# Performance work log

Measured on AMD Instinct MI355X. Metric: run time of the kernel, lower is better.

Reference implementation:

```python
import jax, jax.numpy as jnp
import numpy as np

MARGIN = 0.2
ALPHA = 2.0
BETA = 1.5
ANGLE_THRESHOLD = 30.0
EPS_PD = 1e-6   # F.pairwise_distance eps
EPS_CS = 1e-8   # F.cosine_similarity eps
NEG_INF = -1e30
POS_INF = 1e30


def setup_inputs() -> dict:
    key = jax.random.key(0)
    k1, k2, k3 = jax.random.split(key, 3)
    B, F, A = 4096, 512, 3
    features = jax.random.normal(k1, (B, F), dtype=jnp.float32)
    labels = jax.random.randint(k2, (B,), 0, 256)
    angles = jax.random.uniform(k3, (B, A), dtype=jnp.float32) * 90.0  # degrees
    features_orig = jax.random.normal(jax.random.fold_in(key, 7), (B, F), dtype=jnp.float32)
    return {"features": features, "labels": labels, "angles": angles, "features_orig": features_orig}


def _cosine_sim_matrix(f):
    norms = jnp.linalg.norm(f, axis=1)
    denom = jnp.maximum(norms[:, None] * norms[None, :], EPS_CS)
    return (f @ f.T) / denom


def _forward(features, labels, angles, features_orig):
    B = features.shape[0]
    idx = jnp.arange(B)
    # pairwise angle distances [B,B] (torch.cdist p=2)
    adist = jnp.sqrt(jnp.sum((angles[:, None, :] - angles[None, :, :]) ** 2, axis=-1))
    same = labels[:, None] == labels[None, :]
    same = same & ~jnp.eye(B, dtype=bool)          # exclude self
    diff = labels[:, None] != labels[None, :]
    has_pos = same.any(axis=1)
    has_neg = diff.any(axis=1)
    valid = has_pos & has_neg
    # hardest positive: same label, largest angle difference
    pos_idx = jnp.argmax(jnp.where(same, adist, NEG_INF), axis=1)
    # hardest negative: among diff-label within angle threshold, most similar feature;
    # else diff-label with smallest angle difference
    sim = _cosine_sim_matrix(features)
    similar = diff & (adist < ANGLE_THRESHOLD)
    sim_any = similar.any(axis=1)
    neg_idx_hard = jnp.argmax(jnp.where(similar, sim, NEG_INF), axis=1)
    neg_idx_far = jnp.argmin(jnp.where(diff, adist, POS_INF), axis=1)
    neg_idx = jnp.where(sim_any, neg_idx_hard, neg_idx_far)
    # triplet distances (F.pairwise_distance adds eps to the diff)
    a = features
    p = features[pos_idx]
    n = features[neg_idx]
    pos_d = jnp.linalg.norm(a - p + EPS_PD, axis=1)
    neg_d = jnp.linalg.norm(a - n + EPS_PD, axis=1)
    # angle-based weights (non-differentiable, matches .item() in torch)
    pa = adist[idx, pos_idx]
    na = adist[idx, neg_idx]
    w = jnp.where(pa > 45.0, ALPHA, 1.0) * jnp.where(na < 15.0, BETA, 1.0)
    basic = jax.nn.relu(pos_d - neg_d + MARGIN)
    vmask = valid.astype(features.dtype)
    cnt = jnp.maximum(vmask.sum(), 1.0)
    triplet_loss = jnp.sum(w * basic * vmask) / cnt
    # reconstruction term
    num = jnp.sum(features * features_orig, axis=1)
    den = jnp.maximum(jnp.linalg.norm(features, axis=1) * jnp.linalg.norm(features_orig, axis=1), EPS_CS)
    recon = 1.0 - jnp.mean(num / den)
    return triplet_loss + 0.1 * recon


def reference(features, labels, angles, features_orig):
    return _forward(features, labels, angles, features_orig)
```

## Files before the change

### kernel.cpp

```cpp
#include <hip/hip_runtime.h>
#include <math.h>

#define BN 4096
#define FD 512
#define TT 128
#define TJ 64
#define BK 64
#define NJT (BN / TT)
#define NPAIR (NJT * (NJT + 1) / 2)
#define NBLK (NPAIR * 2)
#define NPC 128

typedef __attribute__((ext_vector_type(8))) __bf16 bf16x8;
typedef __attribute__((ext_vector_type(4))) float floatx4;
typedef unsigned long long u64;

__device__ __forceinline__ float wred_sum(float v) {
#pragma unroll
  for (int m = 1; m < 64; m <<= 1) v += __shfl_xor(v, m, 64);
  return v;
}

__device__ __forceinline__ float dot4(float4 a, float4 b) {
  return a.x * b.x + a.y * b.y + a.z * b.z + a.w * b.w;
}

__device__ __forceinline__ unsigned short f2bf(float x) {
  unsigned u = __float_as_uint(x);
  u += 0x7fffu + ((u >> 16) & 1u);
  return (unsigned short)(u >> 16);
}

__device__ __forceinline__ void load16(const void* g, void* l) {
  __builtin_amdgcn_global_load_lds(
      (const __attribute__((address_space(1))) unsigned int*)g,
      (__attribute__((address_space(3))) unsigned int*)l, 16, 0, 0);
}

__device__ __forceinline__ unsigned ford(float v) {
  unsigned u = __float_as_uint(v);
  return u ^ (((unsigned)((int)u >> 31)) | 0x80000000u);
}

template <int N>
__device__ __forceinline__ int rori(int x) {
  return __builtin_amdgcn_update_dpp(0, x, 0x120 | N, 0xf, 0xf, true);
}
template <int N>
__device__ __forceinline__ u64 ror16_u64(u64 k) {
  unsigned lo = (unsigned)rori<N>((int)(unsigned)k);
  unsigned hi = (unsigned)rori<N>((int)(unsigned)(k >> 32));
  return ((u64)hi << 32) | lo;
}
__device__ __forceinline__ u64 red16_max_u64(u64 k) {
  u64 o;
  o = ror16_u64<1>(k); k = o > k ? o : k;
  o = ror16_u64<2>(k); k = o > k ? o : k;
  o = ror16_u64<4>(k); k = o > k ? o : k;
  o = ror16_u64<8>(k); k = o > k ? o : k;
  return k;
}

__device__ __forceinline__ u64 sx64(u64 v, int m) {
  unsigned lo = (unsigned)__shfl_xor((int)(unsigned)v, m, 64);
  unsigned hi = (unsigned)__shfl_xor((int)(unsigned)(v >> 32), m, 64);
  return ((u64)hi << 32) | lo;
}

__global__ __launch_bounds__(256) void k_prep(const float* __restrict__ f,
                                              const float* __restrict__ fo,
                                              const float* __restrict__ angles,
                                              unsigned short* __restrict__ gb,
                                              float* __restrict__ rowr,
                                              float* __restrict__ ax,
                                              float* __restrict__ ay,
                                              float* __restrict__ az) {
  const int i = blockIdx.x * 4 + (threadIdx.x >> 6);
  const int lane = threadIdx.x & 63;
  const int t = blockIdx.x * 256 + threadIdx.x;
  if (t < BN) {
    ax[t] = angles[t * 3 + 0];
    ay[t] = angles[t * 3 + 1];
    az[t] = angles[t * 3 + 2];
  }
  const float4* fr = (const float4*)(f + (size_t)i * FD);
  const float4* orr = (const float4*)(fo + (size_t)i * FD);
  float4 x0 = fr[lane], x1 = fr[lane + 64];
  float4 y0 = orr[lane], y1 = orr[lane + 64];
  float sff = dot4(x0, x0) + dot4(x1, x1);
  float sfo = dot4(x0, y0) + dot4(x1, y1);
  float soo = dot4(y0, y0) + dot4(y1, y1);
  sff = wred_sum(sff);
  sfo = wred_sum(sfo);
  soo = wred_sum(soo);
  float nf = sqrtf(sff);
  float inv = 1.0f / nf;
  ushort4* gr = (ushort4*)(gb + (size_t)i * FD);
  ushort4 s0, s1;
  s0.x = f2bf(x0.x * inv); s0.y = f2bf(x0.y * inv);
  s0.z = f2bf(x0.z * inv); s0.w = f2bf(x0.w * inv);
  s1.x = f2bf(x1.x * inv); s1.y = f2bf(x1.y * inv);
  s1.z = f2bf(x1.z * inv); s1.w = f2bf(x1.w * inv);
  gr[lane] = s0;
  gr[lane + 64] = s1;
  if (lane == 0) {
    rowr[i] = sfo / fmaxf(nf * sqrtf(soo), 1e-8f);
  }
}

__global__ __launch_bounds__(256, 4) void k_sim(const unsigned short* __restrict__ gb,
                                                const int* __restrict__ labels,
                                                const float* __restrict__ ax,
                                                const float* __restrict__ ay,
                                                const float* __restrict__ az,
                                                u64* __restrict__ pkey) {
  __shared__ unsigned short As[TT * BK];
  __shared__ unsigned short Bs[TJ * BK];
  const int h = blockIdx.x & 1;
  int a = 0, rem = blockIdx.x >> 1;
#pragma unroll 1
  while (rem >= NJT - a) { rem -= NJT - a; a++; }
  const int b = a + rem;
  const int i0 = a * TT;
  const int j0 = b * TT + h * TJ;

  const int tid = threadIdx.x;
  const int w = tid >> 6;
  const int lane = tid & 63;

  floatx4 acc[2][4];
#pragma unroll
  for (int u = 0; u < 2; u++)
#pragma unroll
    for (int v = 0; v < 4; v++) acc[u][v] = (floatx4){0.f, 0.f, 0.f, 0.f};

  const int rp = tid >> 3;
  const int q8 = ((tid & 7) ^ (rp & 7)) * 8;
  const unsigned short* gA[4];
  const unsigned short* gB[2];
  unsigned short* lA[4];
  unsigned short* lB[2];
#pragma unroll
  for (int c = 0; c < 4; c++) {
    gA[c] = gb + (size_t)(i0 + rp + 32 * c) * FD + q8;
    lA[c] = As + (tid + 256 * c) * 8;
  }
#pragma unroll
  for (int c = 0; c < 2; c++) {
    gB[c] = gb + (size_t)(j0 + rp + 32 * c) * FD + q8;
    lB[c] = Bs + (tid + 256 * c) * 8;
  }

  const int m = lane & 15;
  const int arow = w * 32 + m;
  const int brow = m;
  const int g4 = lane >> 4;
  const int l7 = lane & 7;
  const int koff0 = (g4 ^ l7) * 8;
  const int koff1 = ((4 + g4) ^ l7) * 8;

  for (int kc = 0; kc < FD; kc += BK) {
#pragma unroll
    for (int c = 0; c < 4; c++) load16(gA[c] + kc, lA[c]);
#pragma unroll
    for (int c = 0; c < 2; c++) load16(gB[c] + kc, lB[c]);
    __syncthreads();
    bf16x8 af[2], bf[4];
#pragma unroll
    for (int u = 0; u < 2; u++)
      af[u] = *(const bf16x8*)(As + (arow + u * 16) * BK + koff0);
#pragma unroll
    for (int v = 0; v < 4; v++)
      bf[v] = *(const bf16x8*)(Bs + (brow + v * 16) * BK + koff0);
#pragma unroll
    for (int u = 0; u < 2; u++)
#pragma unroll
      for (int v = 0; v < 4; v++)
        acc[u][v] = __builtin_amdgcn_mfma_f32_16x16x32_bf16(af[u], bf[v], acc[u][v], 0, 0, 0);
#pragma unroll
    for (int u = 0; u < 2; u++)
      af[u] = *(const bf16x8*)(As + (arow + u * 16) * BK + koff1);
#pragma unroll
    for (int v = 0; v < 4; v++)
      bf[v] = *(const bf16x8*)(Bs + (brow + v * 16) * BK + koff1);
#pragma unroll
    for (int u = 0; u < 2; u++)
#pragma unroll
      for (int v = 0; v < 4; v++)
        acc[u][v] = __builtin_amdgcn_mfma_f32_16x16x32_bf16(af[u], bf[v], acc[u][v], 0, 0, 0);
    __syncthreads();
  }

  const int quad = lane >> 4;
  const int cx = lane & 15;
  int jc[4], lj[4];
  float jx[4], jy[4], jz[4];
#pragma unroll
  for (int v = 0; v < 4; v++) {
    jc[v] = j0 + v * 16 + cx;
    lj[v] = labels[jc[v]];
    jx[v] = ax[jc[v]];
    jy[v] = ay[jc[v]];
    jz[v] = az[jc[v]];
  }
  const size_t rbase = (size_t)(64 + 2 * b + h) * BN;
  u64 ckey[4] = {0, 0, 0, 0};
#pragma unroll
  for (int u = 0; u < 2; u++) {
#pragma unroll
    for (int reg = 0; reg < 4; reg++) {
      int i = i0 + w * 32 + u * 16 + quad * 4 + reg;
      int li = labels[i];
      float a0 = ax[i], a1 = ay[i], a2 = az[i];
      u64 rkey = 0;
      unsigned ni = (unsigned)(~i);
#pragma unroll
      for (int v = 0; v < 4; v++) {
        float d0 = a0 - jx[v];
        float d1 = a1 - jy[v];
        float d2 = a2 - jz[v];
        float dd = d0 * d0 + d1 * d1 + d2 * d2;
        bool ok = (li != lj[v]) && (dd < 900.0f);
        u64 vh = (u64)ford(acc[u][v][reg]) << 32;
        u64 candR = vh | (unsigned)(~jc[v]);
        if (ok && candR > rkey) rkey = candR;
        u64 candC = vh | ni;
        if (ok && candC > ckey[v]) ckey[v] = candC;
      }
      rkey = red16_max_u64(rkey);
      if (cx == 0) pkey[rbase + i] = rkey;
    }
  }
  if (a != b) {
    const size_t cbase = (size_t)(4 * a + w) * BN;
#pragma unroll
    for (int v = 0; v < 4; v++) {
      u64 k = ckey[v];
      u64 o = sx64(k, 16); if (o > k) k = o;
      o = sx64(k, 32); if (o > k) k = o;
      if (quad == 0) pkey[cbase + jc[v]] = k;
    }
  }
}

__global__ __launch_bounds__(256) void k_final(const float* __restrict__ f,
                                               const int* __restrict__ labels,
                                               const float* __restrict__ ax,
                                               const float* __restrict__ ay,
                                               const float* __restrict__ az,
                                               const u64* __restrict__ pkey,
                                               float* __restrict__ rowc,
                                               float* __restrict__ rowv) {
  const int i = blockIdx.x * 4 + (threadIdx.x >> 6);
  const int lane = threadIdx.x & 63;
  const int li = labels[i];
  const float a0 = ax[i], a1 = ay[i], a2 = az[i];

  u64 keyP = 0;
  u64 keyN = ~0ull;
  const float4* ax4 = (const float4*)ax;
  const float4* ay4 = (const float4*)ay;
  const float4* az4 = (const float4*)az;
  const int4* lb4 = (const int4*)labels;
#pragma unroll
  for (int it = 0; it < 16; it++) {
    int bb = it * 64 + lane;
    float4 X = ax4[bb], Y = ay4[bb], Z = az4[bb];
    int4 L = lb4[bb];
    int jb = bb * 4;
#pragma unroll
    for (int s = 0; s < 4; s++) {
      float xx = s == 0 ? X.x : s == 1 ? X.y : s == 2 ? X.z : X.w;
      float yy = s == 0 ? Y.x : s == 1 ? Y.y : s == 2 ? Y.z : Y.w;
      float zz = s == 0 ? Z.x : s == 1 ? Z.y : s == 2 ? Z.z : Z.w;
      int ll = s == 0 ? L.x : s == 1 ? L.y : s == 2 ? L.z : L.w;
      int j = jb + s;
      float d0 = a0 - xx, d1 = a1 - yy, d2 = a2 - zz;
      float dd = d0 * d0 + d1 * d1 + d2 * d2;
      if (ll == li) {
        u64 kp = ((u64)__float_as_uint(dd) << 32) | (unsigned)(~j);
        if (j != i && kp > keyP) keyP = kp;
      } else {
        u64 kn = ((u64)__float_as_uint(dd) << 32) | (unsigned)j;
        if (kn < keyN) keyN = kn;
      }
    }
  }
  const int t = i >> 7;
  u64 s0 = (lane < 4 * t) ? pkey[(size_t)lane * BN + i] : 0;
  u64 s1 = (lane >= 2 * t) ? pkey[(size_t)(64 + lane) * BN + i] : 0;
  u64 keyS = s0 > s1 ? s0 : s1;
#pragma unroll
  for (int off = 1; off < 64; off <<= 1) {
    u64 o = sx64(keyP, off);
    if (o > keyP) keyP = o;
    o = sx64(keyN, off);
    if (o < keyN) keyN = o;
    o = sx64(keyS, off);
    if (o > keyS) keyS = o;
  }
  bool hp = keyP != 0;
  bool hn = keyN != ~0ull;
  if (!(hp && hn)) {
    if (lane == 0) { rowc[i] = 0.0f; rowv[i] = 0.0f; }
    return;
  }
  bool sim_any = keyS != 0;
  int pos = (int)(~(unsigned)keyP);
  int neg = sim_any ? (int)(~(unsigned)keyS) : (int)(unsigned)keyN;

  const float4* fa = (const float4*)(f + (size_t)i * FD);
  const float4* fp = (const float4*)(f + (size_t)pos * FD);
  const float4* fn = (const float4*)(f + (size_t)neg * FD);
  float sp = 0.0f, sn = 0.0f;
#pragma unroll
  for (int t2 = 0; t2 < 2; t2++) {
    float4 xa = fa[lane + t2 * 64];
    float4 xp = fp[lane + t2 * 64];
    float4 xn = fn[lane + t2 * 64];
    float dp;
    dp = xa.x - xp.x + 1e-6f; sp += dp * dp;
    dp = xa.y - xp.y + 1e-6f; sp += dp * dp;
    dp = xa.z - xp.z + 1e-6f; sp += dp * dp;
    dp = xa.w - xp.w + 1e-6f; sp += dp * dp;
    dp = xa.x - xn.x + 1e-6f; sn += dp * dp;
    dp = xa.y - xn.y + 1e-6f; sn += dp * dp;
    dp = xa.z - xn.z + 1e-6f; sn += dp * dp;
    dp = xa.w - xn.w + 1e-6f; sn += dp * dp;
  }
  sp = wred_sum(sp);
  sn = wred_sum(sn);

  if (lane == 0) {
    float pos_d = sqrtf(sp);
    float neg_d = sqrtf(sn);
    float pa = sqrtf(__uint_as_float((unsigned)(keyP >> 32)));
    float n0 = a0 - ax[neg];
    float n1 = a1 - ay[neg];
    float n2 = a2 - az[neg];
    float na = sqrtf(n0 * n0 + n1 * n1 + n2 * n2);
    float w = (pa > 45.0f ? 2.0f : 1.0f) * (na < 15.0f ? 1.5f : 1.0f);
    float basic = fmaxf(pos_d - neg_d + 0.2f, 0.0f);
    rowc[i] = w * basic;
    rowv[i] = 1.0f;
  }
}

__global__ __launch_bounds__(1024) void k_out(const float* __restrict__ rowc,
                                              const float* __restrict__ rowv,
                                              const float* __restrict__ rowr,
                                              float* __restrict__ out) {
  __shared__ float sc[16], sv[16], sr[16];
  const int t = threadIdx.x;
  float c = 0.0f, v = 0.0f, r = 0.0f;
  for (int i = t; i < BN; i += 1024) {
    c += rowc[i];
    v += rowv[i];
    r += rowr[i];
  }
  c = wred_sum(c);
  v = wred_sum(v);
  r = wred_sum(r);
  const int wid = t >> 6;
  if ((t & 63) == 0) { sc[wid] = c; sv[wid] = v; sr[wid] = r; }
  __syncthreads();
  if (t == 0) {
    float C = 0.0f, V = 0.0f, R = 0.0f;
#pragma unroll
    for (int k = 0; k < 16; k++) { C += sc[k]; V += sv[k]; R += sr[k]; }
    float tri = C / fmaxf(V, 1.0f);
    float recon = 1.0f - R / (float)BN;
    out[0] = tri + 0.1f * recon;
  }
}

extern "C" void kernel_launch(void* const* d_in, const int* in_sizes, int n_in,
                              void* d_out, int out_size, void* d_ws, size_t ws_size,
                              hipStream_t stream) {
  const float* feat = (const float*)d_in[0];
  const int* labels = (const int*)d_in[1];
  const float* angles = (const float*)d_in[2];
  const float* forig = (const float*)d_in[3];
  float* out = (float*)d_out;

  char* ws = (char*)d_ws;
  unsigned short* gb = (unsigned short*)ws;
  size_t off = (size_t)BN * FD * sizeof(unsigned short);
  u64* pkey = (u64*)(ws + off);     off += (size_t)NPC * BN * 8;
  float* rowc = (float*)(ws + off); off += (size_t)BN * 4;
  float* rowv = (float*)(ws + off); off += (size_t)BN * 4;
  float* rowr = (float*)(ws + off); off += (size_t)BN * 4;
  float* ax = (float*)(ws + off);   off += (size_t)BN * 4;
  float* ay = (float*)(ws + off);   off += (size_t)BN * 4;
  float* az = (float*)(ws + off);   off += (size_t)BN * 4;

  k_prep<<<BN / 4, 256, 0, stream>>>(feat, forig, angles, gb, rowr, ax, ay, az);
  k_sim<<<NBLK, 256, 0, stream>>>(gb, labels, ax, ay, az, pkey);
  k_final<<<BN / 4, 256, 0, stream>>>(feat, labels, ax, ay, az, pkey, rowc, rowv);
  k_out<<<1, 1024, 0, stream>>>(rowc, rowv, rowr, out);
}
```

Before: 108.6 us.

## Bucket rows by label, defer negative scan, fuse final reduction into k_final

Builds per-label buckets (a count histogram in k_prep plus a single-block prefix-scan/scatter kernel) so the hardest-positive search in k_final visits only same-label rows instead of all 4096. The nearest-negative full scan now runs only when no similar negative exists, and has_pos/has_neg come from bucket counts. The separate k_out reduction is folded into k_final using per-block partials and a last-block atomic counter. In exchange it adds a memset, a serial single-block kernel launch, global atomics, and scattered gathers of angle data through the bucket indices.

```diff
diff --git a/kernel.cpp b/kernel.cpp
--- a/kernel.cpp
+++ b/kernel.cpp
@@ -10,6 +10,7 @@
 #define NPAIR (NJT * (NJT + 1) / 2)
 #define NBLK (NPAIR * 2)
 #define NPC 128
+#define NFB (BN / 4)
 
 typedef __attribute__((ext_vector_type(8))) __bf16 bf16x8;
 typedef __attribute__((ext_vector_type(4))) float floatx4;
@@ -70,11 +71,13 @@
 __global__ __launch_bounds__(256) void k_prep(const float* __restrict__ f,
                                               const float* __restrict__ fo,
                                               const float* __restrict__ angles,
+                                              const int* __restrict__ labels,
                                               unsigned short* __restrict__ gb,
                                               float* __restrict__ rowr,
                                               float* __restrict__ ax,
                                               float* __restrict__ ay,
-                                              float* __restrict__ az) {
+                                              float* __restrict__ az,
+                                              int* __restrict__ cntP) {
   const int i = blockIdx.x * 4 + (threadIdx.x >> 6);
   const int lane = threadIdx.x & 63;
   const int t = blockIdx.x * 256 + threadIdx.x;
@@ -83,6 +86,7 @@
     ay[t] = angles[t * 3 + 1];
     az[t] = angles[t * 3 + 2];
   }
+  if (lane == 0) atomicAdd(&cntP[labels[i] * 16], 1);
   const float4* fr = (const float4*)(f + (size_t)i * FD);
   const float4* orr = (const float4*)(fo + (size_t)i * FD);
   float4 x0 = fr[lane], x1 = fr[lane + 64];
@@ -108,6 +112,36 @@
   }
 }
 
+__global__ __launch_bounds__(256) void k_bucket(const int* __restrict__ labels,
+                                                const int* __restrict__ cntP,
+                                                int* __restrict__ curP,
+                                                int* __restrict__ offc,
+                                                int* __restrict__ cntc,
+                                                int* __restrict__ bucket) {
+  __shared__ int pre[256];
+  const int tid = threadIdx.x;
+  int c = cntP[tid * 16];
+  pre[tid] = c;
+  __syncthreads();
+#pragma unroll
+  for (int s = 1; s < 256; s <<= 1) {
+    int v = (tid >= s) ? pre[tid - s] : 0;
+    __syncthreads();
+    pre[tid] += v;
+    __syncthreads();
+  }
+  int excl = pre[tid] - c;
+  offc[tid] = excl;
+  cntc[tid] = c;
+  curP[tid * 16] = excl;
+  __syncthreads();
+  for (int i = tid; i < BN; i += 256) {
+    int lab = labels[i];
+    int pos = atomicAdd(&curP[lab * 16], 1);
+    bucket[pos] = i;
+  }
+}
+
 __global__ __launch_bounds__(256, 4) void k_sim(const unsigned short* __restrict__ gb,
                                                 const int* __restrict__ labels,
                                                 const float* __restrict__ ax,
@@ -249,41 +283,33 @@
                                                const float* __restrict__ ay,
                                                const float* __restrict__ az,
                                                const u64* __restrict__ pkey,
-                                               float* __restrict__ rowc,
-                                               float* __restrict__ rowv) {
-  const int i = blockIdx.x * 4 + (threadIdx.x >> 6);
+                                               const float* __restrict__ rowr,
+                                               const int* __restrict__ bucket,
+                                               const int* __restrict__ offc,
+                                               const int* __restrict__ cntc,
+                                               float* __restrict__ blkC,
+                                               float* __restrict__ blkV,
+                                               float* __restrict__ blkR,
+                                               int* __restrict__ counter,
+                                               float* __restrict__ out) {
+  __shared__ float s_c[4], s_v[4], s_r[4];
+  __shared__ int s_go;
+  const int wid = threadIdx.x >> 6;
+  const int i = blockIdx.x * 4 + wid;
   const int lane = threadIdx.x & 63;
   const int li = labels[i];
   const float a0 = ax[i], a1 = ay[i], a2 = az[i];
 
+  const int bc = cntc[li];
+  const int bo = offc[li];
   u64 keyP = 0;
-  u64 keyN = ~0ull;
-  const float4* ax4 = (const float4*)ax;
-  const float4* ay4 = (const float4*)ay;
-  const float4* az4 = (const float4*)az;
-  const int4* lb4 = (const int4*)labels;
-#pragma unroll
-  for (int it = 0; it < 16; it++) {
-    int bb = it * 64 + lane;
-    float4 X = ax4[bb], Y = ay4[bb], Z = az4[bb];
-    int4 L = lb4[bb];
-    int jb = bb * 4;
-#pragma unroll
-    for (int s = 0; s < 4; s++) {
-      float xx = s == 0 ? X.x : s == 1 ? X.y : s == 2 ? X.z : X.w;
-      float yy = s == 0 ? Y.x : s == 1 ? Y.y : s == 2 ? Y.z : Y.w;
-      float zz = s == 0 ? Z.x : s == 1 ? Z.y : s == 2 ? Z.z : Z.w;
-      int ll = s == 0 ? L.x : s == 1 ? L.y : s == 2 ? L.z : L.w;
-      int j = jb + s;
-      float d0 = a0 - xx, d1 = a1 - yy, d2 = a2 - zz;
+  for (int l = lane; l < bc; l += 64) {
+    int j = bucket[bo + l];
+    if (j != i) {
+      float d0 = a0 - ax[j], d1 = a1 - ay[j], d2 = a2 - az[j];
       float dd = d0 * d0 + d1 * d1 + d2 * d2;
-      if (ll == li) {
-        u64 kp = ((u64)__float_as_uint(dd) << 32) | (unsigned)(~j);
-        if (j != i && kp > keyP) keyP = kp;
-      } else {
-        u64 kn = ((u64)__float_as_uint(dd) << 32) | (unsigned)j;
-        if (kn < keyN) keyN = kn;
-      }
+      u64 kp = ((u64)__float_as_uint(dd) << 32) | (unsigned)(~j);
+      if (kp > keyP) keyP = kp;
     }
   }
   const int t = i >> 7;
@@ -294,83 +320,122 @@
   for (int off = 1; off < 64; off <<= 1) {
     u64 o = sx64(keyP, off);
     if (o > keyP) keyP = o;
-    o = sx64(keyN, off);
-    if (o < keyN) keyN = o;
     o = sx64(keyS, off);
     if (o > keyS) keyS = o;
   }
-  bool hp = keyP != 0;
-  bool hn = keyN != ~0ull;
-  if (!(hp && hn)) {
-    if (lane == 0) { rowc[i] = 0.0f; rowv[i] = 0.0f; }
-    return;
-  }
+  bool hp = bc > 1;
+  bool hn = bc < BN;
   bool sim_any = keyS != 0;
-  int pos = (int)(~(unsigned)keyP);
-  int neg = sim_any ? (int)(~(unsigned)keyS) : (int)(unsigned)keyN;
-
-  const float4* fa = (const float4*)(f + (size_t)i * FD);
-  const float4* fp = (const float4*)(f + (size_t)pos * FD);
-  const float4* fn = (const float4*)(f + (size_t)neg * FD);
-  float sp = 0.0f, sn = 0.0f;
-#pragma unroll
-  for (int t2 = 0; t2 < 2; t2++) {
-    float4 xa = fa[lane + t2 * 64];
-    float4 xp = fp[lane + t2 * 64];
-    float4 xn = fn[lane + t2 * 64];
-    float dp;
-    dp = xa.x - xp.x + 1e-6f; sp += dp * dp;
-    dp = xa.y - xp.y + 1e-6f; sp += dp * dp;
-    dp = xa.z - xp.z + 1e-6f; sp += dp * dp;
-    dp = xa.w - xp.w + 1e-6f; sp += dp * dp;
-    dp = xa.x - xn.x + 1e-6f; sn += dp * dp;
-    dp = xa.y - xn.y + 1e-6f; sn += dp * dp;
-    dp = xa.z - xn.z + 1e-6f; sn += dp * dp;
-    dp = xa.w - xn.w + 1e-6f; sn += dp * dp;
-  }
-  sp = wred_sum(sp);
-  sn = wred_sum(sn);
-
+  float rc = 0.0f, rv = 0.0f;
+  if (hp && hn) {
+    int neg;
+    if (sim_any) {
+      neg = (int)(~(unsigned)keyS);
+    } else {
+      u64 keyN = ~0ull;
+      const float4* ax4 = (const float4*)ax;
+      const float4* ay4 = (const float4*)ay;
+      const float4* az4 = (const float4*)az;
+      const int4* lb4 = (const int4*)labels;
+      for (int it = 0; it < 16; it++) {
+        int bb = it * 64 + lane;
+        float4 X = ax4[bb], Y = ay4[bb], Z = az4[bb];
+        int4 L = lb4[bb];
+        int jb = bb * 4;
+#pragma unroll
+        for (int s = 0; s < 4; s++) {
+          float xx = s == 0 ? X.x : s == 1 ? X.y : s == 2 ? X.z : X.w;
+          float yy = s == 0 ? Y.x : s == 1 ? Y.y : s == 2 ? Y.z : Y.w;
+          float zz = s == 0 ? Z.x : s == 1 ? Z.y : s == 2 ? Z.z : Z.w;
+          int ll = s == 0 ? L.x : s == 1 ? L.y : s == 2 ? L.z : L.w;
+          int j = jb + s;
+          if (ll != li) {
+            float d0 = a0 - xx, d1 = a1 - yy, d2 = a2 - zz;
+            float dd = d0 * d0 + d1 * d1 + d2 * d2;
+            u64 kn = ((u64)__float_as_uint(dd) << 32) | (unsigned)j;
+            if (kn < keyN) keyN = kn;
+          }
+        }
+      }
+#pragma unroll
+      for (int off = 1; off < 64; off <<= 1) {
+        u64 o = sx64(keyN, off);
+        if (o < keyN) keyN = o;
+      }
+      neg = (int)(unsigned)keyN;
+    }
+    int pos = (int)(~(unsigned)keyP);
+
+    const float4* fa = (const float4*)(f + (size_t)i * FD);
+    const float4* fp = (const float4*)(f + (size_t)pos * FD);
+    const float4* fn = (const float4*)(f + (size_t)neg * FD);
+    float sp = 0.0f, sn = 0.0f;
+#pragma unroll
+    for (int t2 = 0; t2 < 2; t2++) {
+      float4 xa = fa[lane + t2 * 64];
+      float4 xp = fp[lane + t2 * 64];
+      float4 xn = fn[lane + t2 * 64];
+      float dp;
+      dp = xa.x - xp.x + 1e-6f; sp += dp * dp;
+      dp = xa.y - xp.y + 1e-6f; sp += dp * dp;
+      dp = xa.z - xp.z + 1e-6f; sp += dp * dp;
+      dp = xa.w - xp.w + 1e-6f; sp += dp * dp;
+      dp = xa.x - xn.x + 1e-6f; sn += dp * dp;
+      dp = xa.y - xn.y + 1e-6f; sn += dp * dp;
+      dp = xa.z - xn.z + 1e-6f; sn += dp * dp;
+      dp = xa.w - xn.w + 1e-6f; sn += dp * dp;
+    }
+    sp = wred_sum(sp);
+    sn = wred_sum(sn);
+    if (lane == 0) {
+      float pos_d = sqrtf(sp);
+      float neg_d = sqrtf(sn);
+      float pa = sqrtf(__uint_as_float((unsigned)(keyP >> 32)));
+      float n0 = a0 - ax[neg];
+      float n1 = a1 - ay[neg];
+      float n2 = a2 - az[neg];
+      float na = sqrtf(n0 * n0 + n1 * n1 + n2 * n2);
+      float w = (pa > 45.0f ? 2.0f : 1.0f) * (na < 15.0f ? 1.5f : 1.0f);
+      rc = w * fmaxf(pos_d - neg_d + 0.2f, 0.0f);
+      rv = 1.0f;
+    }
+  }
   if (lane == 0) {
-    float pos_d = sqrtf(sp);
-    float neg_d = sqrtf(sn);
-    float pa = sqrtf(__uint_as_float((unsigned)(keyP >> 32)));
-    float n0 = a0 - ax[neg];
-    float n1 = a1 - ay[neg];
-    float n2 = a2 - az[neg];
-    float na = sqrtf(n0 * n0 + n1 * n1 + n2 * n2);
-    float w = (pa > 45.0f ? 2.0f : 1.0f) * (na < 15.0f ? 1.5f : 1.0f);
-    float basic = fmaxf(pos_d - neg_d + 0.2f, 0.0f);
-    rowc[i] = w * basic;
-    rowv[i] = 1.0f;
-  }
-}
-
-__global__ __launch_bounds__(1024) void k_out(const float* __restrict__ rowc,
-                                              const float* __restrict__ rowv,
-                                              const float* __restrict__ rowr,
-                                              float* __restrict__ out) {
-  __shared__ float sc[16], sv[16], sr[16];
-  const int t = threadIdx.x;
-  float c = 0.0f, v = 0.0f, r = 0.0f;
-  for (int i = t; i < BN; i += 1024) {
-    c += rowc[i];
-    v += rowv[i];
-    r += rowr[i];
-  }
-  c = wred_sum(c);
-  v = wred_sum(v);
-  r = wred_sum(r);
-  const int wid = t >> 6;
-  if ((t & 63) == 0) { sc[wid] = c; sv[wid] = v; sr[wid] = r; }
+    s_c[wid] = rc;
+    s_v[wid] = rv;
+    s_r[wid] = rowr[i];
+  }
   __syncthreads();
-  if (t == 0) {
+  if (threadIdx.x == 0) {
+    blkC[blockIdx.x] = s_c[0] + s_c[1] + s_c[2] + s_c[3];
+    blkV[blockIdx.x] = s_v[0] + s_v[1] + s_v[2] + s_v[3];
+    blkR[blockIdx.x] = s_r[0] + s_r[1] + s_r[2] + s_r[3];
+    __threadfence();
+    int old = atomicAdd(counter, 1);
+    s_go = (old == NFB - 1) ? 1 : 0;
+  }
+  __syncthreads();
+  if (s_go) {
+    __threadfence();
     float C = 0.0f, V = 0.0f, R = 0.0f;
-#pragma unroll
-    for (int k = 0; k < 16; k++) { C += sc[k]; V += sv[k]; R += sr[k]; }
-    float tri = C / fmaxf(V, 1.0f);
-    float recon = 1.0f - R / (float)BN;
-    out[0] = tri + 0.1f * recon;
+    for (int k = threadIdx.x; k < NFB; k += 256) {
+      C += blkC[k];
+      V += blkV[k];
+      R += blkR[k];
+    }
+    C = wred_sum(C);
+    V = wred_sum(V);
+    R = wred_sum(R);
+    if (lane == 0) { s_c[wid] = C; s_v[wid] = V; s_r[wid] = R; }
+    __syncthreads();
+    if (threadIdx.x == 0) {
+      float Ct = s_c[0] + s_c[1] + s_c[2] + s_c[3];
+      float Vt = s_v[0] + s_v[1] + s_v[2] + s_v[3];
+      float Rt = s_r[0] + s_r[1] + s_r[2] + s_r[3];
+      float tri = Ct / fmaxf(Vt, 1.0f);
+      float recon = 1.0f - Rt / (float)BN;
+      out[0] = tri + 0.1f * recon;
+    }
   }
 }
 
@@ -386,16 +451,25 @@
   char* ws = (char*)d_ws;
   unsigned short* gb = (unsigned short*)ws;
   size_t off = (size_t)BN * FD * sizeof(unsigned short);
-  u64* pkey = (u64*)(ws + off);     off += (size_t)NPC * BN * 8;
-  float* rowc = (float*)(ws + off); off += (size_t)BN * 4;
-  float* rowv = (float*)(ws + off); off += (size_t)BN * 4;
+  u64* pkey = (u64*)(ws + off);    off += (size_t)NPC * BN * 8;
   float* rowr = (float*)(ws + off); off += (size_t)BN * 4;
-  float* ax = (float*)(ws + off);   off += (size_t)BN * 4;
-  float* ay = (float*)(ws + off);   off += (size_t)BN * 4;
-  float* az = (float*)(ws + off);   off += (size_t)BN * 4;
-
-  k_prep<<<BN / 4, 256, 0, stream>>>(feat, forig, angles, gb, rowr, ax, ay, az);
+  float* ax = (float*)(ws + off);  off += (size_t)BN * 4;
+  float* ay = (float*)(ws + off);  off += (size_t)BN * 4;
+  float* az = (float*)(ws + off);  off += (size_t)BN * 4;
+  int* cntP = (int*)(ws + off);    off += 256 * 16 * 4;
+  int* counter = (int*)(ws + off); off += 64;
+  int* curP = (int*)(ws + off);    off += 256 * 16 * 4;
+  int* offc = (int*)(ws + off);    off += 256 * 4;
+  int* cntc = (int*)(ws + off);    off += 256 * 4;
+  int* bucket = (int*)(ws + off);  off += (size_t)BN * 4;
+  float* blkC = (float*)(ws + off); off += NFB * 4;
+  float* blkV = (float*)(ws + off); off += NFB * 4;
+  float* blkR = (float*)(ws + off); off += NFB * 4;
+
+  hipMemsetAsync(cntP, 0, 256 * 16 * 4 + 64, stream);
+  k_prep<<<BN / 4, 256, 0, stream>>>(feat, forig, angles, labels, gb, rowr, ax, ay, az, cntP);
+  k_bucket<<<1, 256, 0, stream>>>(labels, cntP, curP, offc, cntc, bucket);
   k_sim<<<NBLK, 256, 0, stream>>>(gb, labels, ax, ay, az, pkey);
-  k_final<<<BN / 4, 256, 0, stream>>>(feat, labels, ax, ay, az, pkey, rowc, rowv);
-  k_out<<<1, 1024, 0, stream>>>(rowc, rowv, rowr, out);
-}
+  k_final<<<NFB, 256, 0, stream>>>(feat, labels, ax, ay, az, pkey, rowr, bucket,
+                                   offc, cntc, blkC, blkV, blkR, counter, out);
+}
```

Result: slower. 142.1 us (+30.8%).
